# Kernel optimization log

Measured on AMD Instinct MI355X. Metric: run time of the kernel, lower is better.

## Reference

```python
import jax, jax.numpy as jnp
import numpy as np

BINS = 10
IGNORE_INDEX = -100


def setup_inputs() -> dict:
    key = jax.random.key(0)
    k1, k2 = jax.random.split(key)
    B, C = 4096, 32000
    y_pred = jax.random.normal(k1, (B, C), dtype=jnp.float32)
    y_true = jax.random.randint(k2, (B,), 0, C, dtype=jnp.int64)
    return {"y_pred": y_pred, "y_true": y_true}


def reference(y_pred, y_true):
    # y_pred: [B, C] logits, y_true: [B] labels
    C = y_pred.shape[-1]
    # stable softmax -> gather prob of true class (log_softmax == log(softmax))
    logp = jax.nn.log_softmax(y_pred, axis=-1)                      # [B, C]
    safe_idx = jnp.clip(y_true, 0, C - 1)
    y_logprob = jnp.take_along_axis(logp, safe_idx[:, None], 1)[:, 0]  # [B]
    y_prob = jnp.exp(y_logprob)                                     # [B]

    valid = (y_true != IGNORE_INDEX)                                # [B] bool
    num_labels = valid.sum().astype(y_pred.dtype)

    # gradient norm g = 1 - p, binned into BINS equal-width bins over [0, 1)
    g = 1.0 - y_prob
    edges = jnp.arange(BINS + 1, dtype=y_pred.dtype) / BINS         # histogram edges
    # bin i satisfies edges[i] <= g < edges[i+1]
    bin_idx = jnp.searchsorted(edges, g, side="right") - 1          # [B]
    in_range = (bin_idx >= 0) & (bin_idx < BINS) & valid
    seg = jnp.where(in_range, bin_idx, BINS)                        # overflow bin BINS

    counts = jax.ops.segment_sum(
        jnp.ones_like(g), seg, num_segments=BINS + 1)[:BINS]        # [BINS]
    nonempty = counts > 0
    wpb = jnp.where(nonempty, num_labels / jnp.where(nonempty, counts, 1.0), 0.0)
    n = nonempty.sum().astype(y_pred.dtype)
    wpb = wpb / jnp.maximum(n, 1.0)
    wpb_pad = jnp.concatenate([wpb, jnp.zeros((1,), y_pred.dtype)])  # overflow -> 0
    weights = jax.lax.stop_gradient(wpb_pad[seg])                   # [B]

    # masked log-prob (ignored positions contribute 0; weights already 0 there)
    y_logprob = jnp.where(valid, y_logprob, 0.0)
    loss = -(weights * y_logprob)                                   # [B]
    return loss.sum() / num_labels                                  # reduction='mean'
```

## Files before the change

### kernel.cpp

```cpp
#include <hip/hip_runtime.h>
#include <math.h>

#define BINS 10
#define IGNORE_INDEX (-100)

typedef float fvec4 __attribute__((ext_vector_type(4)));

__device__ __forceinline__ float safe_expf(float d) {
    return (d != d || d == -INFINITY) ? 0.0f : __expf(d);
}

__device__ __forceinline__ void acc4(fvec4 v, float& m, float& s) {
    float vm = fmaxf(fmaxf(v.x, v.y), fmaxf(v.z, v.w));
    if (vm > m) { s *= safe_expf(m - vm); m = vm; }
    s += (__expf(v.x - m) + __expf(v.y - m)) + (__expf(v.z - m) + __expf(v.w - m));
}

__global__ __launch_bounds__(256) void ghmc_row_kernel(
    const float* __restrict__ y_pred,
    const int*   __restrict__ y_true,
    float*       __restrict__ logprob,
    int*         __restrict__ seg,
    int C)
{
    const int row = blockIdx.x;
    const float* rp = y_pred + (size_t)row * (size_t)C;
    const int tid = threadIdx.x;
    const int nthreads = blockDim.x;

    const int label = y_true[row];
    const int cidx  = label < 0 ? 0 : (label >= C ? C - 1 : label);
    const float xt  = rp[cidx];

    float m0 = -INFINITY, s0 = 0.0f;
    float m1 = -INFINITY, s1 = 0.0f;

    const int n4 = C >> 2;
    const fvec4* rp4 = reinterpret_cast<const fvec4*>(rp);

    int i = tid;
    for (; i + nthreads < n4; i += 2 * nthreads) {
        fvec4 a = __builtin_nontemporal_load(&rp4[i]);
        fvec4 b = __builtin_nontemporal_load(&rp4[i + nthreads]);
        acc4(a, m0, s0);
        acc4(b, m1, s1);
    }
    for (; i < n4; i += nthreads) {
        fvec4 a = __builtin_nontemporal_load(&rp4[i]);
        acc4(a, m0, s0);
    }
    for (int j = (n4 << 2) + tid; j < C; j += nthreads) {
        float v = rp[j];
        if (v > m0) { s0 *= safe_expf(m0 - v); m0 = v; }
        s0 += __expf(v - m0);
    }

    {
        float nm = fmaxf(m0, m1);
        s0 = s0 * safe_expf(m0 - nm) + s1 * safe_expf(m1 - nm);
        m0 = nm;
    }

    #pragma unroll
    for (int off = 32; off >= 1; off >>= 1) {
        float om = __shfl_xor(m0, off);
        float os = __shfl_xor(s0, off);
        float nm = fmaxf(m0, om);
        s0 = s0 * safe_expf(m0 - nm) + os * safe_expf(om - nm);
        m0 = nm;
    }

    __shared__ float sm[4], ss[4];
    const int wave = tid >> 6, lane = tid & 63;
    if (lane == 0) { sm[wave] = m0; ss[wave] = s0; }
    __syncthreads();

    if (tid == 0) {
        float M = sm[0], S = ss[0];
        #pragma unroll
        for (int w = 1; w < 4; ++w) {
            float om = sm[w], os = ss[w];
            float nm = fmaxf(M, om);
            S = S * safe_expf(M - nm) + os * safe_expf(om - nm);
            M = nm;
        }
        float lp = xt - M - logf(S);
        logprob[row] = lp;

        float p = __expf(lp);
        float g = 1.0f - p;

        int bin = -1;
        #pragma unroll
        for (int k = 0; k <= BINS; ++k) {
            float edge = (float)k / (float)BINS;
            if (edge <= g) bin = k;
        }
        const bool valid = (label != IGNORE_INDEX);
        const bool in_range = (bin >= 0) && (bin < BINS) && valid;
        seg[row] = in_range ? bin : BINS;
    }
}

__global__ __launch_bounds__(1024) void ghmc_finalize_kernel(
    const int*   __restrict__ y_true,
    const float* __restrict__ logprob,
    const int*   __restrict__ seg,
    float*       __restrict__ out,
    int B)
{
    const int tid = threadIdx.x;
    const int wave = tid >> 6, lane = tid & 63;
    const int NW = 16;

    __shared__ int s_counts[BINS + 1];
    if (tid < BINS + 1) s_counts[tid] = 0;
    __syncthreads();

    int nl = 0;
    for (int i = tid; i < B; i += blockDim.x) {
        const int label = y_true[i];
        nl += (label != IGNORE_INDEX) ? 1 : 0;
        const int sg = seg[i];
        if (sg < BINS) atomicAdd(&s_counts[sg], 1);
    }
    #pragma unroll
    for (int off = 32; off >= 1; off >>= 1) nl += __shfl_xor(nl, off);

    __shared__ int snl[NW];
    if (lane == 0) snl[wave] = nl;
    __syncthreads();

    __shared__ float wpb[BINS + 1];
    __shared__ float s_num_labels;
    if (tid == 0) {
        int NL = 0;
        #pragma unroll
        for (int w = 0; w < NW; ++w) NL += snl[w];
        const float num_labels = (float)NL;
        s_num_labels = num_labels;
        int n = 0;
        #pragma unroll
        for (int k = 0; k < BINS; ++k) n += (s_counts[k] > 0) ? 1 : 0;
        const float nf = fmaxf((float)n, 1.0f);
        #pragma unroll
        for (int k = 0; k < BINS; ++k) {
            float w = (s_counts[k] > 0) ? (num_labels / (float)s_counts[k]) : 0.0f;
            wpb[k] = w / nf;
        }
        wpb[BINS] = 0.0f;
    }
    __syncthreads();

    float acc = 0.0f;
    for (int i = tid; i < B; i += blockDim.x) {
        const int label = y_true[i];
        const bool valid = (label != IGNORE_INDEX);
        const float lp = valid ? logprob[i] : 0.0f;
        acc += -(wpb[seg[i]] * lp);
    }
    #pragma unroll
    for (int off = 32; off >= 1; off >>= 1) acc += __shfl_xor(acc, off);

    __shared__ float sacc[NW];
    if (lane == 0) sacc[wave] = acc;
    __syncthreads();
    if (tid == 0) {
        float total = 0.0f;
        #pragma unroll
        for (int w = 0; w < NW; ++w) total += sacc[w];
        out[0] = total / s_num_labels;
    }
}

extern "C" void kernel_launch(void* const* d_in, const int* in_sizes, int n_in,
                              void* d_out, int out_size, void* d_ws, size_t ws_size,
                              hipStream_t stream) {
    const float* y_pred = (const float*)d_in[0];
    const int*   y_true = (const int*)d_in[1];
    const int B = in_sizes[1];
    const int C = (int)(in_sizes[0] / (size_t)in_sizes[1]);
    float* out = (float*)d_out;

    char* ws = (char*)d_ws;
    float* logprob = (float*)ws;
    int*   seg     = (int*)(ws + (size_t)B * sizeof(float));

    ghmc_row_kernel<<<B, 256, 0, stream>>>(y_pred, y_true, logprob, seg, C);
    ghmc_finalize_kernel<<<1, 1024, 0, stream>>>(y_true, logprob, seg, out, B);
}
```

Measured before the change: 91.31 us.

## Accumulate per-bin counts and logprob sums via sharded atomics; unroll row loop 4x

The row kernel no longer writes per-row logprob and segment arrays. It atomically adds counts, per-bin log-prob sums and the valid-label count into 64 sharded slots, using the fact that the loss equals a sum over bins of weight times per-bin log-prob sum. The finalize kernel shrinks to a single wave that reduces the shards, and a memset is added to zero them. The streaming loop also keeps four independent max/sum accumulators instead of two for more memory-level parallelism. Float atomics make the summation order nondeterministic.

```diff
diff --git a/kernel.cpp b/kernel.cpp
--- a/kernel.cpp
+++ b/kernel.cpp
@@ -3,6 +3,8 @@
 
 #define BINS 10
 #define IGNORE_INDEX (-100)
+#define NSHADOW 64
+#define SH_STRIDE 16
 
 typedef float fvec4 __attribute__((ext_vector_type(4)));
 
@@ -19,8 +21,9 @@
 __global__ __launch_bounds__(256) void ghmc_row_kernel(
     const float* __restrict__ y_pred,
     const int*   __restrict__ y_true,
-    float*       __restrict__ logprob,
-    int*         __restrict__ seg,
+    int*         __restrict__ counts_sh,
+    float*       __restrict__ binsum_sh,
+    int*         __restrict__ nl_sh,
     int C)
 {
     const int row = blockIdx.x;
@@ -34,16 +37,22 @@
 
     float m0 = -INFINITY, s0 = 0.0f;
     float m1 = -INFINITY, s1 = 0.0f;
+    float m2 = -INFINITY, s2 = 0.0f;
+    float m3 = -INFINITY, s3 = 0.0f;
 
     const int n4 = C >> 2;
     const fvec4* rp4 = reinterpret_cast<const fvec4*>(rp);
 
     int i = tid;
-    for (; i + nthreads < n4; i += 2 * nthreads) {
+    for (; i + 3 * nthreads < n4; i += 4 * nthreads) {
         fvec4 a = __builtin_nontemporal_load(&rp4[i]);
         fvec4 b = __builtin_nontemporal_load(&rp4[i + nthreads]);
+        fvec4 c = __builtin_nontemporal_load(&rp4[i + 2 * nthreads]);
+        fvec4 d = __builtin_nontemporal_load(&rp4[i + 3 * nthreads]);
         acc4(a, m0, s0);
         acc4(b, m1, s1);
+        acc4(c, m2, s2);
+        acc4(d, m3, s3);
     }
     for (; i < n4; i += nthreads) {
         fvec4 a = __builtin_nontemporal_load(&rp4[i]);
@@ -58,6 +67,12 @@
     {
         float nm = fmaxf(m0, m1);
         s0 = s0 * safe_expf(m0 - nm) + s1 * safe_expf(m1 - nm);
+        m0 = nm;
+        nm = fmaxf(m2, m3);
+        s2 = s2 * safe_expf(m2 - nm) + s3 * safe_expf(m3 - nm);
+        m2 = nm;
+        nm = fmaxf(m0, m2);
+        s0 = s0 * safe_expf(m0 - nm) + s2 * safe_expf(m2 - nm);
         m0 = nm;
     }
 
@@ -85,7 +100,6 @@
             M = nm;
         }
         float lp = xt - M - logf(S);
-        logprob[row] = lp;
 
         float p = __expf(lp);
         float g = 1.0f - p;
@@ -98,78 +112,61 @@
         }
         const bool valid = (label != IGNORE_INDEX);
         const bool in_range = (bin >= 0) && (bin < BINS) && valid;
-        seg[row] = in_range ? bin : BINS;
+
+        const int sh = row & (NSHADOW - 1);
+        if (valid) atomicAdd(&nl_sh[sh], 1);
+        if (in_range) {
+            atomicAdd(&counts_sh[sh * SH_STRIDE + bin], 1);
+            atomicAdd(&binsum_sh[sh * SH_STRIDE + bin], lp);
+        }
     }
 }
 
-__global__ __launch_bounds__(1024) void ghmc_finalize_kernel(
-    const int*   __restrict__ y_true,
-    const float* __restrict__ logprob,
-    const int*   __restrict__ seg,
-    float*       __restrict__ out,
-    int B)
+__global__ __launch_bounds__(64) void ghmc_finalize_kernel(
+    const int*   __restrict__ counts_sh,
+    const float* __restrict__ binsum_sh,
+    const int*   __restrict__ nl_sh,
+    float*       __restrict__ out)
 {
-    const int tid = threadIdx.x;
-    const int wave = tid >> 6, lane = tid & 63;
-    const int NW = 16;
+    const int lane = threadIdx.x;
 
-    __shared__ int s_counts[BINS + 1];
-    if (tid < BINS + 1) s_counts[tid] = 0;
+    __shared__ int   s_counts[BINS];
+    __shared__ float s_binsum[BINS];
+    __shared__ int   s_nl;
+
+    if (lane < BINS) {
+        int c = 0;
+        float bs = 0.0f;
+        #pragma unroll 4
+        for (int s = 0; s < NSHADOW; ++s) {
+            c  += counts_sh[s * SH_STRIDE + lane];
+            bs += binsum_sh[s * SH_STRIDE + lane];
+        }
+        s_counts[lane] = c;
+        s_binsum[lane] = bs;
+    }
+    if (lane == 63) {
+        int nl = 0;
+        #pragma unroll 4
+        for (int s = 0; s < NSHADOW; ++s) nl += nl_sh[s];
+        s_nl = nl;
+    }
     __syncthreads();
 
-    int nl = 0;
-    for (int i = tid; i < B; i += blockDim.x) {
-        const int label = y_true[i];
-        nl += (label != IGNORE_INDEX) ? 1 : 0;
-        const int sg = seg[i];
-        if (sg < BINS) atomicAdd(&s_counts[sg], 1);
-    }
-    #pragma unroll
-    for (int off = 32; off >= 1; off >>= 1) nl += __shfl_xor(nl, off);
-
-    __shared__ int snl[NW];
-    if (lane == 0) snl[wave] = nl;
-    __syncthreads();
-
-    __shared__ float wpb[BINS + 1];
-    __shared__ float s_num_labels;
-    if (tid == 0) {
-        int NL = 0;
-        #pragma unroll
-        for (int w = 0; w < NW; ++w) NL += snl[w];
-        const float num_labels = (float)NL;
-        s_num_labels = num_labels;
+    if (lane == 0) {
+        const float num_labels = (float)s_nl;
         int n = 0;
         #pragma unroll
         for (int k = 0; k < BINS; ++k) n += (s_counts[k] > 0) ? 1 : 0;
         const float nf = fmaxf((float)n, 1.0f);
+        float total = 0.0f;
         #pragma unroll
         for (int k = 0; k < BINS; ++k) {
             float w = (s_counts[k] > 0) ? (num_labels / (float)s_counts[k]) : 0.0f;
-            wpb[k] = w / nf;
+            w /= nf;
+            total += w * s_binsum[k];
         }
-        wpb[BINS] = 0.0f;
-    }
-    __syncthreads();
-
-    float acc = 0.0f;
-    for (int i = tid; i < B; i += blockDim.x) {
-        const int label = y_true[i];
-        const bool valid = (label != IGNORE_INDEX);
-        const float lp = valid ? logprob[i] : 0.0f;
-        acc += -(wpb[seg[i]] * lp);
-    }
-    #pragma unroll
-    for (int off = 32; off >= 1; off >>= 1) acc += __shfl_xor(acc, off);
-
-    __shared__ float sacc[NW];
-    if (lane == 0) sacc[wave] = acc;
-    __syncthreads();
-    if (tid == 0) {
-        float total = 0.0f;
-        #pragma unroll
-        for (int w = 0; w < NW; ++w) total += sacc[w];
-        out[0] = total / s_num_labels;
+        out[0] = -total / num_labels;
     }
 }
 
@@ -183,9 +180,12 @@
     float* out = (float*)d_out;
 
     char* ws = (char*)d_ws;
-    float* logprob = (float*)ws;
-    int*   seg     = (int*)(ws + (size_t)B * sizeof(float));
+    int*   counts_sh = (int*)ws;
+    float* binsum_sh = (float*)(ws + NSHADOW * SH_STRIDE * 4);
+    int*   nl_sh     = (int*)(ws + 2 * NSHADOW * SH_STRIDE * 4);
+    const size_t stats_bytes = 2 * NSHADOW * SH_STRIDE * 4 + NSHADOW * 4;
 
-    ghmc_row_kernel<<<B, 256, 0, stream>>>(y_pred, y_true, logprob, seg, C);
-    ghmc_finalize_kernel<<<1, 1024, 0, stream>>>(y_true, logprob, seg, out, B);
+    hipMemsetAsync(ws, 0, stats_bytes, stream);
+    ghmc_row_kernel<<<B, 256, 0, stream>>>(y_pred, y_true, counts_sh, binsum_sh, nl_sh, C);
+    ghmc_finalize_kernel<<<1, 64, 0, stream>>>(counts_sh, binsum_sh, nl_sh, out);
 }
```

Result: slower. 108.4 us (+18.7%).

## Fuse finalize into row kernel via global atomics and last-block reduction

Applied to the files above, without the earlier changes.

Removes the separate single-block finalize kernel. Each row block now atomically updates global bin counts and the valid-label count, and the last block to finish, detected through an atomic ticket counter, computes the bin weights and the final weighted sum using vectorized loads. A tiny init kernel zeroes the counters each call. This trades one launch plus a re-read of the labels for global atomics and a serialized tail in one block, and the tail now runs with 256 threads instead of 1024.

```diff
diff --git a/kernel.cpp b/kernel.cpp
--- a/kernel.cpp
+++ b/kernel.cpp
@@ -5,6 +5,7 @@
 #define IGNORE_INDEX (-100)
 
 typedef float fvec4 __attribute__((ext_vector_type(4)));
+typedef int   ivec4 __attribute__((ext_vector_type(4)));
 
 __device__ __forceinline__ float safe_expf(float d) {
     return (d != d || d == -INFINITY) ? 0.0f : __expf(d);
@@ -16,12 +17,18 @@
     s += (__expf(v.x - m) + __expf(v.y - m)) + (__expf(v.z - m) + __expf(v.w - m));
 }
 
+__global__ __launch_bounds__(64) void ghmc_init_kernel(int* stats) {
+    if (threadIdx.x < 16) stats[threadIdx.x] = 0;
+}
+
 __global__ __launch_bounds__(256) void ghmc_row_kernel(
     const float* __restrict__ y_pred,
     const int*   __restrict__ y_true,
+    int*         __restrict__ stats,
     float*       __restrict__ logprob,
     int*         __restrict__ seg,
-    int C)
+    float*       __restrict__ out,
+    int C, int B)
 {
     const int row = blockIdx.x;
     const float* rp = y_pred + (size_t)row * (size_t)C;
@@ -99,53 +106,37 @@
         const bool valid = (label != IGNORE_INDEX);
         const bool in_range = (bin >= 0) && (bin < BINS) && valid;
         seg[row] = in_range ? bin : BINS;
+        if (valid)    atomicAdd(&stats[11], 1);
+        if (in_range) atomicAdd(&stats[bin], 1);
     }
-}
-
-__global__ __launch_bounds__(1024) void ghmc_finalize_kernel(
-    const int*   __restrict__ y_true,
-    const float* __restrict__ logprob,
-    const int*   __restrict__ seg,
-    float*       __restrict__ out,
-    int B)
-{
-    const int tid = threadIdx.x;
-    const int wave = tid >> 6, lane = tid & 63;
-    const int NW = 16;
-
-    __shared__ int s_counts[BINS + 1];
-    if (tid < BINS + 1) s_counts[tid] = 0;
     __syncthreads();
 
-    int nl = 0;
-    for (int i = tid; i < B; i += blockDim.x) {
-        const int label = y_true[i];
-        nl += (label != IGNORE_INDEX) ? 1 : 0;
-        const int sg = seg[i];
-        if (sg < BINS) atomicAdd(&s_counts[sg], 1);
+    __shared__ int s_last;
+    if (tid == 0) {
+        __threadfence();
+        int old = atomicAdd(&stats[12], 1);
+        s_last = (old == gridDim.x - 1) ? 1 : 0;
     }
-    #pragma unroll
-    for (int off = 32; off >= 1; off >>= 1) nl += __shfl_xor(nl, off);
+    __syncthreads();
+    if (!s_last) return;
 
-    __shared__ int snl[NW];
-    if (lane == 0) snl[wave] = nl;
-    __syncthreads();
+    __threadfence();
 
     __shared__ float wpb[BINS + 1];
     __shared__ float s_num_labels;
     if (tid == 0) {
-        int NL = 0;
+        int cnt[BINS];
         #pragma unroll
-        for (int w = 0; w < NW; ++w) NL += snl[w];
-        const float num_labels = (float)NL;
+        for (int k = 0; k < BINS; ++k) cnt[k] = stats[k];
+        const float num_labels = (float)stats[11];
         s_num_labels = num_labels;
         int n = 0;
         #pragma unroll
-        for (int k = 0; k < BINS; ++k) n += (s_counts[k] > 0) ? 1 : 0;
+        for (int k = 0; k < BINS; ++k) n += (cnt[k] > 0) ? 1 : 0;
         const float nf = fmaxf((float)n, 1.0f);
         #pragma unroll
         for (int k = 0; k < BINS; ++k) {
-            float w = (s_counts[k] > 0) ? (num_labels / (float)s_counts[k]) : 0.0f;
+            float w = (cnt[k] > 0) ? (num_labels / (float)cnt[k]) : 0.0f;
             wpb[k] = w / nf;
         }
         wpb[BINS] = 0.0f;
@@ -153,24 +144,26 @@
     __syncthreads();
 
     float acc = 0.0f;
-    for (int i = tid; i < B; i += blockDim.x) {
-        const int label = y_true[i];
-        const bool valid = (label != IGNORE_INDEX);
-        const float lp = valid ? logprob[i] : 0.0f;
-        acc += -(wpb[seg[i]] * lp);
+    const int nv = B >> 2;
+    const ivec4* sg4 = reinterpret_cast<const ivec4*>(seg);
+    const fvec4* lp4 = reinterpret_cast<const fvec4*>(logprob);
+    for (int ii = tid; ii < nv; ii += nthreads) {
+        ivec4 sg = sg4[ii];
+        fvec4 lp = lp4[ii];
+        #pragma unroll
+        for (int k = 0; k < 4; ++k) acc += -(wpb[sg[k]] * lp[k]);
     }
+    for (int ii = (nv << 2) + tid; ii < B; ii += nthreads)
+        acc += -(wpb[seg[ii]] * logprob[ii]);
+
     #pragma unroll
     for (int off = 32; off >= 1; off >>= 1) acc += __shfl_xor(acc, off);
 
-    __shared__ float sacc[NW];
+    __shared__ float sacc[4];
     if (lane == 0) sacc[wave] = acc;
     __syncthreads();
-    if (tid == 0) {
-        float total = 0.0f;
-        #pragma unroll
-        for (int w = 0; w < NW; ++w) total += sacc[w];
-        out[0] = total / s_num_labels;
-    }
+    if (tid == 0)
+        out[0] = (sacc[0] + sacc[1] + sacc[2] + sacc[3]) / s_num_labels;
 }
 
 extern "C" void kernel_launch(void* const* d_in, const int* in_sizes, int n_in,
@@ -183,9 +176,10 @@
     float* out = (float*)d_out;
 
     char* ws = (char*)d_ws;
-    float* logprob = (float*)ws;
-    int*   seg     = (int*)(ws + (size_t)B * sizeof(float));
+    int*   stats   = (int*)ws;
+    float* logprob = (float*)(ws + 64);
+    int*   seg     = (int*)(ws + 64 + (size_t)B * sizeof(float));
 
-    ghmc_row_kernel<<<B, 256, 0, stream>>>(y_pred, y_true, logprob, seg, C);
-    ghmc_finalize_kernel<<<1, 1024, 0, stream>>>(y_true, logprob, seg, out, B);
+    ghmc_init_kernel<<<1, 64, 0, stream>>>(stats);
+    ghmc_row_kernel<<<B, 256, 0, stream>>>(y_pred, y_true, stats, logprob, seg, out, C, B);
 }
```

Result: slower. 282.2 us (+209.0%).
